# Performance work log

Hardware: AMD Instinct MI355X
Metric: run time of the kernel (lower is better)

## Reference

```python
import jax, jax.numpy as jnp
import numpy as np

E = 64          # moe_num_experts
H = 1024        # hidden_size
F = 2816        # per_expert_ff_dim
T = 4096        # total tokens (equal split: 64 per expert)


def setup_inputs() -> dict:
    key = jax.random.key(0)
    k1, k2, k3, k4 = jax.random.split(key, 4)
    s = 1.0 / np.sqrt(H)
    return {
        "x": jax.random.normal(k1, (T, H), dtype=jnp.float32),
        "tokens_per_expert": jnp.full((E,), T // E, dtype=jnp.int32),
        "w1": jax.random.normal(k2, (E * F, H), dtype=jnp.float32) * s,
        "w3": jax.random.normal(k3, (E * F, H), dtype=jnp.float32) * s,
        "w2": jax.random.normal(k4, (E * F, H), dtype=jnp.float32) * s,
    }


def reference(x, tokens_per_expert, w1, w3, w2):
    # Tokens are grouped contiguously per expert with an equal split,
    # so the variable-size grouped GEMM (gg.ops.gmm) reduces to a batched einsum.
    tpe = x.shape[0] // E
    xg = x.reshape(E, tpe, H)            # [E, t, h]
    w1e = w1.reshape(E, F, H)
    w3e = w3.reshape(E, F, H)
    w2e = w2.reshape(E, F, H)
    # gmm(x, w1, trans_b=True): per-expert x @ w1[e].T
    h1 = jnp.einsum("eth,efh->etf", xg, w1e)   # [E, t, f]
    h3 = jnp.einsum("eth,efh->etf", xg, w3e)   # [E, t, f]
    gated = jax.nn.silu(h1) * h3               # SwiGLU
    # gmm(gated, w2): per-expert gated @ w2[e]  ([t,f] @ [f,h])
    out = jnp.einsum("etf,efh->eth", gated, w2e)
    return out.reshape(-1, H)
```

## Files before the change

kernel.cpp:

```cpp
#include <hip/hip_runtime.h>
#include <hip/hip_bf16.h>

#define NE   64
#define NH   1024
#define NF   2816
#define TPE  64
#define BK   64
#define PITCH 72

typedef __attribute__((ext_vector_type(8))) short bf16x8;
typedef __attribute__((ext_vector_type(4))) float f32x4;

__device__ __forceinline__ ushort f2bf(float f) {
    union { float f; unsigned u; } v; v.f = f;
    unsigned r = v.u + 0x7fffu + ((v.u >> 16) & 1u);
    return (ushort)(r >> 16);
}

__global__ __launch_bounds__(256, 2)
void k1_gate(const float* __restrict__ x,
             const float* __restrict__ w1,
             const float* __restrict__ w3,
             ushort* __restrict__ g) {
    __shared__ ushort lA [64 * PITCH];
    __shared__ ushort lB1[64 * PITCH];
    __shared__ ushort lB3[64 * PITCH];

    const int jt   = blockIdx.x;
    const int e    = blockIdx.y;
    const int tid  = threadIdx.x;
    const int lane = tid & 63;
    const int wid  = tid >> 6;

    const float* xA = x  + (size_t)e * TPE * NH;
    const float* B1 = w1 + ((size_t)e * NF + (size_t)jt * 64) * NH;
    const float* B3 = w3 + ((size_t)e * NF + (size_t)jt * 64) * NH;

    f32x4 acc1[4], acc3[4];
    for (int nf = 0; nf < 4; ++nf) {
        acc1[nf] = f32x4{0.f, 0.f, 0.f, 0.f};
        acc3[nf] = f32x4{0.f, 0.f, 0.f, 0.f};
    }

    for (int kt = 0; kt < NH / BK; ++kt) {
        __syncthreads();
        #pragma unroll
        for (int r = 0; r < 4; ++r) {
            const int q   = tid + r * 256;
            const int row = q >> 4;
            const int k4  = (q & 15) * 4;
            const float4 va = *(const float4*)(xA + (size_t)row * NH + kt * BK + k4);
            const float4 v1 = *(const float4*)(B1 + (size_t)row * NH + kt * BK + k4);
            const float4 v3 = *(const float4*)(B3 + (size_t)row * NH + kt * BK + k4);
            ushort4 a, b, c;
            a.x = f2bf(va.x); a.y = f2bf(va.y); a.z = f2bf(va.z); a.w = f2bf(va.w);
            b.x = f2bf(v1.x); b.y = f2bf(v1.y); b.z = f2bf(v1.z); b.w = f2bf(v1.w);
            c.x = f2bf(v3.x); c.y = f2bf(v3.y); c.z = f2bf(v3.z); c.w = f2bf(v3.w);
            *(ushort4*)(&lA [row * PITCH + k4]) = a;
            *(ushort4*)(&lB1[row * PITCH + k4]) = b;
            *(ushort4*)(&lB3[row * PITCH + k4]) = c;
        }
        __syncthreads();

        const int mrow = wid * 16 + (lane & 15);
        #pragma unroll
        for (int ks = 0; ks < 2; ++ks) {
            const int koff = ks * 32 + ((lane >> 4) * 8);
            const bf16x8 af = *(const bf16x8*)(&lA[mrow * PITCH + koff]);
            #pragma unroll
            for (int nf = 0; nf < 4; ++nf) {
                const int brow = (nf * 16 + (lane & 15)) * PITCH + koff;
                const bf16x8 b1 = *(const bf16x8*)(&lB1[brow]);
                acc1[nf] = __builtin_amdgcn_mfma_f32_16x16x32_bf16(af, b1, acc1[nf], 0, 0, 0);
                const bf16x8 b3 = *(const bf16x8*)(&lB3[brow]);
                acc3[nf] = __builtin_amdgcn_mfma_f32_16x16x32_bf16(af, b3, acc3[nf], 0, 0, 0);
            }
        }
    }

    #pragma unroll
    for (int nf = 0; nf < 4; ++nf) {
        #pragma unroll
        for (int i = 0; i < 4; ++i) {
            const float h1v = acc1[nf][i];
            const float h3v = acc3[nf][i];
            const float s   = (h1v / (1.f + __expf(-h1v))) * h3v;
            const int row = wid * 16 + ((lane >> 4) * 4) + i;
            const int col = jt * 64 + nf * 16 + (lane & 15);
            const size_t t = (size_t)e * TPE + row;
            g[t * NF + col] = f2bf(s);
        }
    }
}

__global__ __launch_bounds__(256, 2)
void k2_down(const ushort* __restrict__ g,
             const float* __restrict__ w2,
             float* __restrict__ out) {
    __shared__ ushort lA[64 * PITCH];
    __shared__ ushort lB[64 * PITCH];

    const int jt   = blockIdx.x;
    const int e    = blockIdx.y;
    const int tid  = threadIdx.x;
    const int lane = tid & 63;
    const int wid  = tid >> 6;

    const ushort* A = g  + (size_t)e * TPE * NF;
    const float*  B = w2 + (size_t)e * NF * NH + (size_t)jt * 64;
    float* O = out + (size_t)e * TPE * NH + (size_t)jt * 64;

    f32x4 acc[4];
    for (int nf = 0; nf < 4; ++nf) acc[nf] = f32x4{0.f, 0.f, 0.f, 0.f};

    for (int kt = 0; kt < NF / BK; ++kt) {
        __syncthreads();
        #pragma unroll
        for (int r = 0; r < 2; ++r) {
            const int q   = tid + r * 256;
            const int row = q >> 3;
            const int k8  = (q & 7) * 8;
            *(bf16x8*)(&lA[row * PITCH + k8]) =
                *(const bf16x8*)(A + (size_t)row * NF + kt * BK + k8);
        }
        {
            const int n  = tid & 63;
            const int kq = (tid >> 6) * 4;
            #pragma unroll
            for (int r = 0; r < 4; ++r) {
                const int ks = kq + r * 16;
                const size_t base = (size_t)(kt * BK + ks) * NH + n;
                const float f0 = B[base];
                const float f1 = B[base + NH];
                const float f2 = B[base + 2 * (size_t)NH];
                const float f3 = B[base + 3 * (size_t)NH];
                ushort4 b;
                b.x = f2bf(f0); b.y = f2bf(f1); b.z = f2bf(f2); b.w = f2bf(f3);
                *(ushort4*)(&lB[n * PITCH + ks]) = b;
            }
        }
        __syncthreads();

        const int mrow = wid * 16 + (lane & 15);
        #pragma unroll
        for (int ks = 0; ks < 2; ++ks) {
            const int koff = ks * 32 + ((lane >> 4) * 8);
            const bf16x8 af = *(const bf16x8*)(&lA[mrow * PITCH + koff]);
            #pragma unroll
            for (int nf = 0; nf < 4; ++nf) {
                const bf16x8 bfr = *(const bf16x8*)(&lB[(nf * 16 + (lane & 15)) * PITCH + koff]);
                acc[nf] = __builtin_amdgcn_mfma_f32_16x16x32_bf16(af, bfr, acc[nf], 0, 0, 0);
            }
        }
    }

    #pragma unroll
    for (int nf = 0; nf < 4; ++nf) {
        #pragma unroll
        for (int i = 0; i < 4; ++i) {
            const int row = wid * 16 + ((lane >> 4) * 4) + i;
            const int col = nf * 16 + (lane & 15);
            O[(size_t)row * NH + col] = acc[nf][i];
        }
    }
}

extern "C" void kernel_launch(void* const* d_in, const int* in_sizes, int n_in,
                              void* d_out, int out_size, void* d_ws, size_t ws_size,
                              hipStream_t stream) {
    const float* x  = (const float*)d_in[0];
    const float* w1 = (const float*)d_in[2];
    const float* w3 = (const float*)d_in[3];
    const float* w2 = (const float*)d_in[4];
    float* out = (float*)d_out;
    ushort* gated = (ushort*)d_ws;

    dim3 g1(NF / 64, NE);
    k1_gate<<<g1, dim3(256), 0, stream>>>(x, w1, w3, gated);

    dim3 g2(NH / 64, NE);
    k2_down<<<g2, dim3(256), 0, stream>>>(gated, w2, out);
}
```

Measured before the change: 531.8 us.

## Stage fp32 gate tiles via direct global-to-LDS loads with XOR swizzle

The gate/up kernel now copies fp32 tiles of x, w1 and w3 straight into LDS with global_load_lds instead of loading into registers, converting to bf16 and storing. LDS holds fp32 tiles laid out with an XOR swizzle to avoid bank conflicts, and the bf16 conversion moves to the point where MFMA operands are read. The aim is to take the register round-trip and conversion out of the load phase. In exchange, LDS use roughly doubles, every MFMA operand is converted repeatedly, and launch bounds now ask for 3 blocks per CU.

Measured after the change: 440.6 us. 17.2% less time.

```diff
diff --git a/kernel.cpp b/kernel.cpp
--- a/kernel.cpp
+++ b/kernel.cpp
@@ -17,63 +17,83 @@
     return (ushort)(r >> 16);
 }
 
-__global__ __launch_bounds__(256, 2)
+__device__ __forceinline__ bf16x8 cvt8(f32x4 lo, f32x4 hi) {
+    bf16x8 r;
+    #pragma unroll
+    for (int j = 0; j < 4; ++j) {
+        r[j]     = (short)f2bf(lo[j]);
+        r[4 + j] = (short)f2bf(hi[j]);
+    }
+    return r;
+}
+
+#define GLOAD16(gsrc, ldst)                                                          \
+    __builtin_amdgcn_global_load_lds(                                                \
+        (const __attribute__((address_space(1))) void*)(gsrc),                       \
+        (__attribute__((address_space(3))) void*)(ldst), 16, 0, 0)
+
+__global__ __launch_bounds__(256, 3)
 void k1_gate(const float* __restrict__ x,
              const float* __restrict__ w1,
              const float* __restrict__ w3,
              ushort* __restrict__ g) {
-    __shared__ ushort lA [64 * PITCH];
-    __shared__ ushort lB1[64 * PITCH];
-    __shared__ ushort lB3[64 * PITCH];
+    __shared__ float lA [64 * 64];
+    __shared__ float lB1[64 * 64];
+    __shared__ float lB3[64 * 64];
 
     const int jt   = blockIdx.x;
     const int e    = blockIdx.y;
     const int tid  = threadIdx.x;
     const int lane = tid & 63;
     const int wid  = tid >> 6;
+    const int m15  = lane & 15;
+    const int hi   = lane >> 4;
 
     const float* xA = x  + (size_t)e * TPE * NH;
     const float* B1 = w1 + ((size_t)e * NF + (size_t)jt * 64) * NH;
     const float* B3 = w3 + ((size_t)e * NF + (size_t)jt * 64) * NH;
 
     f32x4 acc1[4], acc3[4];
+    #pragma unroll
     for (int nf = 0; nf < 4; ++nf) {
         acc1[nf] = f32x4{0.f, 0.f, 0.f, 0.f};
         acc3[nf] = f32x4{0.f, 0.f, 0.f, 0.f};
     }
 
+    const int mrow = wid * 16 + m15;
+
     for (int kt = 0; kt < NH / BK; ++kt) {
         __syncthreads();
         #pragma unroll
         for (int r = 0; r < 4; ++r) {
-            const int q   = tid + r * 256;
-            const int row = q >> 4;
-            const int k4  = (q & 15) * 4;
-            const float4 va = *(const float4*)(xA + (size_t)row * NH + kt * BK + k4);
-            const float4 v1 = *(const float4*)(B1 + (size_t)row * NH + kt * BK + k4);
-            const float4 v3 = *(const float4*)(B3 + (size_t)row * NH + kt * BK + k4);
-            ushort4 a, b, c;
-            a.x = f2bf(va.x); a.y = f2bf(va.y); a.z = f2bf(va.z); a.w = f2bf(va.w);
-            b.x = f2bf(v1.x); b.y = f2bf(v1.y); b.z = f2bf(v1.z); b.w = f2bf(v1.w);
-            c.x = f2bf(v3.x); c.y = f2bf(v3.y); c.z = f2bf(v3.z); c.w = f2bf(v3.w);
-            *(ushort4*)(&lA [row * PITCH + k4]) = a;
-            *(ushort4*)(&lB1[row * PITCH + k4]) = b;
-            *(ushort4*)(&lB3[row * PITCH + k4]) = c;
-        }
-        __syncthreads();
-
-        const int mrow = wid * 16 + (lane & 15);
+            const int s    = r * 256 + tid;
+            const int row  = s >> 4;
+            const int c16  = (s & 15) ^ (row & 15);
+            const size_t goff = (size_t)row * NH + (size_t)kt * BK + c16 * 4;
+            const int lbase = (s & ~63) * 4;
+            GLOAD16(xA + goff, lA  + lbase);
+            GLOAD16(B1 + goff, lB1 + lbase);
+            GLOAD16(B3 + goff, lB3 + lbase);
+        }
+        __syncthreads();
+
         #pragma unroll
         for (int ks = 0; ks < 2; ++ks) {
-            const int koff = ks * 32 + ((lane >> 4) * 8);
-            const bf16x8 af = *(const bf16x8*)(&lA[mrow * PITCH + koff]);
+            const int c0 = ks * 8 + hi * 2;
+            const int sa0 = (c0    ) ^ m15;
+            const int sa1 = (c0 + 1) ^ m15;
+            const f32x4 a0 = *(const f32x4*)&lA[mrow * 64 + sa0 * 4];
+            const f32x4 a1 = *(const f32x4*)&lA[mrow * 64 + sa1 * 4];
+            const bf16x8 af = cvt8(a0, a1);
             #pragma unroll
             for (int nf = 0; nf < 4; ++nf) {
-                const int brow = (nf * 16 + (lane & 15)) * PITCH + koff;
-                const bf16x8 b1 = *(const bf16x8*)(&lB1[brow]);
-                acc1[nf] = __builtin_amdgcn_mfma_f32_16x16x32_bf16(af, b1, acc1[nf], 0, 0, 0);
-                const bf16x8 b3 = *(const bf16x8*)(&lB3[brow]);
-                acc3[nf] = __builtin_amdgcn_mfma_f32_16x16x32_bf16(af, b3, acc3[nf], 0, 0, 0);
+                const int brow = nf * 16 + m15;
+                const f32x4 p0 = *(const f32x4*)&lB1[brow * 64 + sa0 * 4];
+                const f32x4 p1 = *(const f32x4*)&lB1[brow * 64 + sa1 * 4];
+                acc1[nf] = __builtin_amdgcn_mfma_f32_16x16x32_bf16(af, cvt8(p0, p1), acc1[nf], 0, 0, 0);
+                const f32x4 q0 = *(const f32x4*)&lB3[brow * 64 + sa0 * 4];
+                const f32x4 q1 = *(const f32x4*)&lB3[brow * 64 + sa1 * 4];
+                acc3[nf] = __builtin_amdgcn_mfma_f32_16x16x32_bf16(af, cvt8(q0, q1), acc3[nf], 0, 0, 0);
             }
         }
     }
@@ -85,8 +105,8 @@
             const float h1v = acc1[nf][i];
             const float h3v = acc3[nf][i];
             const float s   = (h1v / (1.f + __expf(-h1v))) * h3v;
-            const int row = wid * 16 + ((lane >> 4) * 4) + i;
-            const int col = jt * 64 + nf * 16 + (lane & 15);
+            const int row = wid * 16 + (hi * 4) + i;
+            const int col = jt * 64 + nf * 16 + m15;
             const size_t t = (size_t)e * TPE + row;
             g[t * NF + col] = f2bf(s);
         }
```
